# Kernel tuning notes

Hardware: AMD Instinct MI355X
Metric: run time of the kernel (lower is better)

The kernel has to match this reference:

```python
import jax, jax.numpy as jnp
import numpy as np

D_MODEL, D_K, D_V = 1024, 128, 128
B, S = 4, 4096

def setup_inputs() -> dict:
    key = jax.random.key(0)
    ks = jax.random.split(key, 9)
    sq = 1.0 / np.sqrt(D_MODEL)
    return {
        "q": jax.random.normal(ks[0], (B, S, D_MODEL), jnp.float32),
        "k": jax.random.normal(ks[1], (B, S, D_MODEL), jnp.float32),
        "v": jax.random.normal(ks[2], (B, S, D_MODEL), jnp.float32),
        "wq": jax.random.uniform(ks[3], (D_MODEL, D_K), jnp.float32, -sq, sq),
        "bq": jax.random.uniform(ks[4], (D_K,), jnp.float32, -sq, sq),
        "wk": jax.random.uniform(ks[5], (D_MODEL, D_K), jnp.float32, -sq, sq),
        "bk": jax.random.uniform(ks[6], (D_K,), jnp.float32, -sq, sq),
        "wv": jax.random.uniform(ks[7], (D_MODEL, D_V), jnp.float32, -sq, sq),
        "bv": jax.random.uniform(ks[8], (D_V,), jnp.float32, -sq, sq),
    }

def reference(q, k, v, wq, bq, wk, bk, wv, bv):
    scale = 1.0 / jnp.sqrt(jnp.asarray(D_K, q.dtype))
    qp = q @ wq + bq            # [B,S,Dk]
    kp = k @ wk + bk            # [B,S,Dk]
    vp = v @ wv + bv            # [B,S,Dv]
    scores = jnp.einsum('bqd,bkd->bqk', qp, kp) * scale  # [B,S,S]
    attn = jax.nn.softmax(scores, axis=-1)
    return jnp.einsum('bqk,bkd->bqd', attn, vp)          # [B,S,Dv]
```

## Files before the change

kernel.cpp:

```cpp
#include <hip/hip_runtime.h>
#include <stdint.h>

#define DM 1024
#define DK 128
#define SEQ 4096
#define NB 4
#define NSPLIT 4
#define KSPAN (SEQ / NSPLIT)
#define NQT (SEQ / 128)

typedef float f32x4 __attribute__((ext_vector_type(4)));
typedef float f32x16 __attribute__((ext_vector_type(16)));
typedef __bf16 bf16x8 __attribute__((ext_vector_type(8)));
typedef unsigned short u16x8 __attribute__((ext_vector_type(8)));
typedef unsigned short u16x4 __attribute__((ext_vector_type(4)));

__device__ __forceinline__ unsigned short f2bf(float f) {
    unsigned int u = __builtin_bit_cast(unsigned int, f);
    u += 0x7fffu + ((u >> 16) & 1u);
    return (unsigned short)(u >> 16);
}
__device__ __forceinline__ float bf2f(unsigned short h) {
    unsigned int u = ((unsigned int)h) << 16;
    return __builtin_bit_cast(float, u);
}
__device__ __forceinline__ f32x4 mfma16(u16x8 a, u16x8 b, f32x4 c) {
    return __builtin_amdgcn_mfma_f32_16x16x32_bf16(
        __builtin_bit_cast(bf16x8, a), __builtin_bit_cast(bf16x8, b), c, 0, 0, 0);
}
__device__ __forceinline__ f32x16 mfma32(u16x8 a, u16x8 b, f32x16 c) {
    return __builtin_amdgcn_mfma_f32_32x32x16_bf16(
        __builtin_bit_cast(bf16x8, a), __builtin_bit_cast(bf16x8, b), c, 0, 0, 0);
}

__device__ __forceinline__ bf16x8 cvt84(f32x4 lo, f32x4 hi) {
    bf16x8 r;
    r[0] = (__bf16)lo[0]; r[1] = (__bf16)lo[1]; r[2] = (__bf16)lo[2]; r[3] = (__bf16)lo[3];
    r[4] = (__bf16)hi[0]; r[5] = (__bf16)hi[1]; r[6] = (__bf16)hi[2]; r[7] = (__bf16)hi[3];
    return r;
}

__device__ __forceinline__ void gll16(const void* g, void* l) {
    __builtin_amdgcn_global_load_lds(
        (const __attribute__((address_space(1))) unsigned int*)(uintptr_t)g,
        (__attribute__((address_space(3))) unsigned int*)(uintptr_t)l,
        16, 0, 0);
}

__global__ __launch_bounds__(256) void wt_kernel(
        const float* __restrict__ wq, const float* __restrict__ wk,
        const float* __restrict__ wv, unsigned short* __restrict__ wT) {
    __shared__ unsigned short T[64 * 72];
    const int kt = blockIdx.x, dt = blockIdx.y, mat = blockIdx.z;
    const float* src = (mat == 0) ? wq : (mat == 1 ? wk : wv);
    const int tid = threadIdx.x;
    const int rb = tid >> 4, c4 = (tid & 15) * 4;
    float4 x[4];
#pragma unroll
    for (int i = 0; i < 4; i++)
        x[i] = *(const float4*)&src[(size_t)(kt * 64 + i * 16 + rb) * DK + dt * 64 + c4];
#pragma unroll
    for (int i = 0; i < 4; i++) {
        const int row = i * 16 + rb;
        T[(c4 + 0) * 72 + row] = f2bf(x[i].x);
        T[(c4 + 1) * 72 + row] = f2bf(x[i].y);
        T[(c4 + 2) * 72 + row] = f2bf(x[i].z);
        T[(c4 + 3) * 72 + row] = f2bf(x[i].w);
    }
    __syncthreads();
    const int dl = tid >> 2, ks0 = (tid & 3) * 16;
    unsigned short* dst = wT + (size_t)mat * DM * DK + (size_t)(dt * 64 + dl) * DM + kt * 64 + ks0;
#pragma unroll
    for (int j = 0; j < 2; j++)
        *(u16x8*)&dst[8 * j] = *(const u16x8*)&T[dl * 72 + ks0 + 8 * j];
}

__global__ __launch_bounds__(256)
void proj_kernel(
        const float* __restrict__ qin, const float* __restrict__ kin,
        const float* __restrict__ vin, const unsigned short* __restrict__ wT,
        const float* __restrict__ bq, const float* __restrict__ bk,
        const float* __restrict__ bv,
        unsigned short* __restrict__ qp, unsigned short* __restrict__ kp,
        unsigned short* __restrict__ vpT) {
    __shared__ __align__(16) char smem[64 * 64 * 4 + 128 * 64 * 2];
    float* Xs = (float*)smem;
    unsigned short* Ws = (unsigned short*)(smem + 64 * 64 * 4);

    const int y = blockIdx.y;
    const float* X = (y == 0) ? qin : (y == 1 ? kin : vin);
    const unsigned short* WTm = wT + (size_t)y * (DM * DK);
    const float* bias = (y == 0) ? bq : (y == 1 ? bk : bv);

    const int tid = threadIdx.x;
    const int w = tid >> 6, lane = tid & 63, l16 = lane & 15, quad = lane >> 4;
    const int t0 = blockIdx.x * 64;

    const int lr4 = lane >> 4, h16 = lane & 15;
    const int lr8 = lane >> 3, h8 = lane & 7;
    const float* xsrc[4];
    const unsigned short* wsrc[4];
    float* xdst[4];
    unsigned short* wdst[4];
#pragma unroll
    for (int i = 0; i < 4; i++) {
        const int xrow = w * 16 + i * 4 + lr4;
        const int xcol = (((h16 >> 1) ^ (xrow & 7)) << 3) |
                         (((h16 & 1) ^ ((xrow >> 3) & 1)) << 2);
        xsrc[i] = X + (size_t)(t0 + xrow) * DM + xcol;
        xdst[i] = Xs + (w * 16 + i * 4) * 64;
        const int wrow = w * 32 + i * 8 + lr8;
        const int wcol = (h8 ^ lr8) << 3;
        wsrc[i] = WTm + (size_t)wrow * DM + wcol;
        wdst[i] = Ws + (w * 32 + i * 8) * 64;
    }

    f32x4 zero = {0.f, 0.f, 0.f, 0.f};
    f32x4 acc[4][2];
#pragma unroll
    for (int mf = 0; mf < 4; mf++)
#pragma unroll
        for (int nf = 0; nf < 2; nf++) acc[mf][nf] = zero;

#pragma unroll
    for (int i = 0; i < 4; i++) { gll16(xsrc[i], xdst[i]); gll16(wsrc[i], wdst[i]); }

    const int swz = l16 & 7, h3 = (l16 >> 3) & 1;
    for (int t = 0; t < 16; ++t) {
        __syncthreads();
#pragma unroll
        for (int ks = 0; ks < 2; ks++) {
            const int ca = ((ks << 2) | quad) ^ swz;
            bf16x8 av[4];
            u16x8 bvf[2];
#pragma unroll
            for (int mf = 0; mf < 4; mf++) {
                const float* ap = &Xs[(l16 + 16 * mf) * 64 + ca * 8];
                f32x4 lo = *(const f32x4*)(ap + 4 * h3);
                f32x4 hi = *(const f32x4*)(ap + 4 * (h3 ^ 1));
                av[mf] = cvt84(lo, hi);
            }
#pragma unroll
            for (int nf = 0; nf < 2; nf++)
                bvf[nf] = *(const u16x8*)&Ws[(32 * w + 16 * nf + l16) * 64 + ca * 8];
#pragma unroll
            for (int mf = 0; mf < 4; mf++)
#pragma unroll
                for (int nf = 0; nf < 2; nf++)
                    acc[mf][nf] = __builtin_amdgcn_mfma_f32_16x16x32_bf16(
                        av[mf], __builtin_bit_cast(bf16x8, bvf[nf]), acc[mf][nf], 0, 0, 0);
        }
        __syncthreads();
        if (t < 15) {
#pragma unroll
            for (int i = 0; i < 4; i++) {
                xsrc[i] += 64;
                wsrc[i] += 64;
                gll16(xsrc[i], xdst[i]);
                gll16(wsrc[i], wdst[i]);
            }
        }
    }

    if (y < 2) {
        unsigned short* outp = y ? kp : qp;
#pragma unroll
        for (int nf = 0; nf < 2; nf++) {
            const int n = l16 + 32 * w + 16 * nf;
            const float bb = bias[n];
#pragma unroll
            for (int mf = 0; mf < 4; mf++)
#pragma unroll
                for (int r = 0; r < 4; r++)
                    outp[(size_t)(t0 + 16 * mf + quad * 4 + r) * DK + n] = f2bf(acc[mf][nf][r] + bb);
        }
    } else {
        __syncthreads();
        unsigned short* Tb = (unsigned short*)smem;
#pragma unroll
        for (int nf = 0; nf < 2; nf++) {
            const int d = l16 + 32 * w + 16 * nf;
            const float bb = bias[d];
#pragma unroll
            for (int mf = 0; mf < 4; mf++)
#pragma unroll
                for (int r = 0; r < 4; r++)
                    Tb[d * 72 + 16 * mf + quad * 4 + r] = f2bf(acc[mf][nf][r] + bb);
        }
        __syncthreads();
        const int d2 = tid >> 1, ts = (tid & 1) * 32;
        const int b2 = t0 >> 12, tl0 = t0 & (SEQ - 1);
#pragma unroll
        for (int j = 0; j < 4; j++)
            *(u16x8*)&vpT[((size_t)(b2 * DK + d2)) * SEQ + tl0 + ts + 8 * j] =
                *(const u16x8*)&Tb[d2 * 72 + ts + 8 * j];
    }
}

__global__ __launch_bounds__(256)
__attribute__((amdgpu_waves_per_eu(2, 2)))
void attn_part_kernel(
        const unsigned short* __restrict__ qp, const unsigned short* __restrict__ kp,
        const unsigned short* __restrict__ vpT,
        unsigned short* __restrict__ Opart, float* __restrict__ Lw) {
    __shared__ unsigned short Ks[64 * 136];
    __shared__ unsigned short Vs[128 * 72];

    const int tid = threadIdx.x;
    const int w = tid >> 6, lane = tid & 63, l32 = lane & 31, h = lane >> 5;
    const int qt = blockIdx.x, pi = blockIdx.y, b = blockIdx.z;
    const int q0 = qt * 128;
    const int kbase = pi * KSPAN;
    const float csc = 0.08838834764831845f * 1.4426950408889634f;

    u16x8 qf[8];
    {
        const unsigned short* qrow = qp + (size_t)(b * SEQ + q0 + 32 * w + l32) * DK + 8 * h;
#pragma unroll
        for (int c = 0; c < 8; c++) qf[c] = *(const u16x8*)&qrow[16 * c];
    }

    f32x16 oacc[4];
#pragma unroll
    for (int i = 0; i < 4; i++)
#pragma unroll
        for (int j = 0; j < 16; j++) oacc[i][j] = 0.f;
    float l_acc = 0.f;

    const int krow = tid >> 2, kch = (tid & 3) * 8;
    const int vrow = tid >> 1, voff = (tid & 1) * 8;
    uint4 kbuf[4], vbuf[4];
    {
        const unsigned short* kg = kp + (size_t)(b * SEQ + kbase + krow) * DK + kch;
        const unsigned short* vg = vpT + (size_t)(b * DK + vrow) * SEQ + kbase + voff;
#pragma unroll
        for (int i = 0; i < 4; i++) {
            kbuf[i] = *(const uint4*)&kg[32 * i];
            vbuf[i] = *(const uint4*)&vg[16 * i];
        }
    }

    for (int it = 0; it < KSPAN / 64; it++) {
        __syncthreads();
#pragma unroll
        for (int i = 0; i < 4; i++) {
            *(u16x8*)&Ks[krow * 136 + kch + 32 * i] = __builtin_bit_cast(u16x8, kbuf[i]);
            *(u16x8*)&Vs[vrow * 72 + voff + 16 * i] = __builtin_bit_cast(u16x8, vbuf[i]);
        }
        __syncthreads();
        if (it + 1 < KSPAN / 64) {
            const int kn = kbase + (it + 1) * 64;
            const unsigned short* kg = kp + (size_t)(b * SEQ + kn + krow) * DK + kch;
            const unsigned short* vg = vpT + (size_t)(b * DK + vrow) * SEQ + kn + voff;
#pragma unroll
            for (int i = 0; i < 4; i++) {
                kbuf[i] = *(const uint4*)&kg[32 * i];
                vbuf[i] = *(const uint4*)&vg[16 * i];
            }
        }
        f32x16 sacc[2];
#pragma unroll
        for (int kb = 0; kb < 2; kb++)
#pragma unroll
            for (int j = 0; j < 16; j++) sacc[kb][j] = 0.f;
#pragma unroll
        for (int c = 0; c < 8; c++)
#pragma unroll
            for (int kb = 0; kb < 2; kb++) {
                u16x8 kf = *(const u16x8*)&Ks[(l32 + 32 * kb) * 136 + 16 * c + 8 * h];
                sacc[kb] = mfma32(kf, qf[c], sacc[kb]);
            }
        unsigned int pp[16];
#pragma unroll
        for (int kb = 0; kb < 2; kb++)
#pragma unroll
            for (int r2 = 0; r2 < 8; r2++) {
                float p0 = exp2f(sacc[kb][2 * r2] * csc);
                float p1 = exp2f(sacc[kb][2 * r2 + 1] * csc);
                l_acc += p0 + p1;
                pp[kb * 8 + r2] = (unsigned int)f2bf(p0) | ((unsigned int)f2bf(p1) << 16);
            }
#pragma unroll
        for (int c = 0; c < 4; c++) {
            const int bs = (c >> 1) * 8 + (c & 1) * 4;
            unsigned int o0 = pp[bs], o1 = pp[bs + 1], o2 = pp[bs + 2], o3 = pp[bs + 3];
            unsigned int x0 = __shfl_xor(o0, 32), x1 = __shfl_xor(o1, 32);
            unsigned int x2 = __shfl_xor(o2, 32), x3 = __shfl_xor(o3, 32);
            uint4 af;
            af.x = h ? x2 : o0;
            af.y = h ? x3 : o1;
            af.z = h ? o2 : x0;
            af.w = h ? o3 : x1;
            u16x8 afr = __builtin_bit_cast(u16x8, af);
#pragma unroll
            for (int db = 0; db < 4; db++) {
                u16x8 vf = *(const u16x8*)&Vs[(32 * db + l32) * 72 + 16 * c + 8 * h];
                oacc[db] = mfma32(afr, vf, oacc[db]);
            }
        }
    }
    float l_tot = l_acc + __shfl_xor(l_acc, 32);
    if (lane < 32)
        Lw[(size_t)(b * NSPLIT + pi) * SEQ + q0 + 32 * w + l32] = l_tot;
    float rl[16];
#pragma unroll
    for (int r = 0; r < 16; r++) {
        int qr = (r & 3) + 8 * (r >> 2) + 4 * h;
        rl[r] = 1.f / __shfl(l_tot, qr);
    }
    unsigned short* ob = Opart + ((size_t)((b * NSPLIT + pi) * NQT + qt)) * 16384 + (size_t)tid * 64;
#pragma unroll
    for (int db = 0; db < 4; db++) {
        u16x8 s0, s1;
#pragma unroll
        for (int j = 0; j < 8; j++) {
            s0[j] = f2bf(oacc[db][j] * rl[j]);
            s1[j] = f2bf(oacc[db][8 + j] * rl[8 + j]);
        }
        *(u16x8*)&ob[db * 16] = s0;
        *(u16x8*)&ob[db * 16 + 8] = s1;
    }
}

__global__ __launch_bounds__(256) void attn_combine_kernel(
        const unsigned short* __restrict__ Opart, const float* __restrict__ Lw,
        float* __restrict__ out) {
    __shared__ float Ls[NSPLIT * 128];
    const int tid = threadIdx.x;
    const int w = tid >> 6, lane = tid & 63, l32 = lane & 31, h = lane >> 5;
    const int qt = blockIdx.x, b = blockIdx.y, z = blockIdx.z;
    const int q0 = qt * 128;
    for (int i = tid; i < NSPLIT * 128; i += 256) {
        int pi = i >> 7, ql = i & 127;
        Ls[i] = Lw[(size_t)(b * NSPLIT + pi) * SEQ + q0 + ql];
    }
    __syncthreads();
    int qlr[16];
    float inv[16];
#pragma unroll
    for (int r = 0; r < 16; r++) {
        qlr[r] = 32 * w + (r & 3) + 8 * (r >> 2) + 4 * h;
        float s = 0.f;
#pragma unroll
        for (int pi = 0; pi < NSPLIT; pi++) s += Ls[pi * 128 + qlr[r]];
        inv[r] = 1.f / s;
    }
    float acc[32];
#pragma unroll
    for (int i = 0; i < 32; i++) acc[i] = 0.f;
#pragma unroll
    for (int pi = 0; pi < NSPLIT; pi++) {
        float wr[16];
#pragma unroll
        for (int r = 0; r < 16; r++) wr[r] = Ls[pi * 128 + qlr[r]] * inv[r];
        const unsigned short* ob =
            Opart + ((size_t)((b * NSPLIT + pi) * NQT + qt)) * 16384 + (size_t)tid * 64;
#pragma unroll
        for (int j = 0; j < 2; j++) {
            const int db = 2 * z + j;
#pragma unroll
            for (int hf = 0; hf < 2; hf++) {
                u16x8 v8 = *(const u16x8*)&ob[db * 16 + 8 * hf];
#pragma unroll
                for (int jj = 0; jj < 8; jj++)
                    acc[j * 16 + 8 * hf + jj] += wr[8 * hf + jj] * bf2f(v8[jj]);
            }
        }
    }
#pragma unroll
    for (int j = 0; j < 2; j++) {
        const int db = 2 * z + j;
#pragma unroll
        for (int r = 0; r < 16; r++)
            out[(size_t)(b * SEQ + q0 + qlr[r]) * DK + 32 * db + l32] = acc[j * 16 + r];
    }
}

extern "C" void kernel_launch(void* const* d_in, const int* in_sizes, int n_in,
                              void* d_out, int out_size, void* d_ws, size_t ws_size,
                              hipStream_t stream) {
    const float* q  = (const float*)d_in[0];
    const float* k  = (const float*)d_in[1];
    const float* v  = (const float*)d_in[2];
    const float* wq = (const float*)d_in[3];
    const float* bq = (const float*)d_in[4];
    const float* wk = (const float*)d_in[5];
    const float* bk = (const float*)d_in[6];
    const float* wv = (const float*)d_in[7];
    const float* bv = (const float*)d_in[8];
    float* out = (float*)d_out;

    char* ws = (char*)d_ws;
    unsigned short* wT    = (unsigned short*)(ws);
    unsigned short* qp    = (unsigned short*)(ws + (1u << 20));
    unsigned short* kpb   = (unsigned short*)(ws + (5u << 20));
    unsigned short* vpT   = (unsigned short*)(ws + (9u << 20));
    unsigned short* Opart = (unsigned short*)(ws + (13u << 20));
    float* Lw             = (float*)(ws + (29u << 20));

    hipLaunchKernelGGL(wt_kernel, dim3(16, 2, 3), dim3(256), 0, stream, wq, wk, wv, wT);
    hipLaunchKernelGGL(proj_kernel, dim3(256, 3), dim3(256), 0, stream,
                       q, k, v, wT, bq, bk, bv, qp, kpb, vpT);
    hipLaunchKernelGGL(attn_part_kernel, dim3(NQT, NSPLIT, NB), dim3(256), 0, stream,
                       qp, kpb, vpT, Opart, Lw);
    hipLaunchKernelGGL(attn_combine_kernel, dim3(NQT, NB, 2), dim3(256), 0, stream,
                       Opart, Lw, out);
}
```

Baseline: 286.9 us.

## Double-buffer LDS tiles in projection GEMM to overlap loads with MFMA

```diff
diff --git a/kernel.cpp b/kernel.cpp
--- a/kernel.cpp
+++ b/kernel.cpp
@@ -83,9 +83,7 @@
         const float* __restrict__ bv,
         unsigned short* __restrict__ qp, unsigned short* __restrict__ kp,
         unsigned short* __restrict__ vpT) {
-    __shared__ __align__(16) char smem[64 * 64 * 4 + 128 * 64 * 2];
-    float* Xs = (float*)smem;
-    unsigned short* Ws = (unsigned short*)(smem + 64 * 64 * 4);
+    __shared__ __align__(16) char smem[2 * 32768];
 
     const int y = blockIdx.y;
     const float* X = (y == 0) ? qin : (y == 1 ? kin : vin);
@@ -100,20 +98,30 @@
     const int lr8 = lane >> 3, h8 = lane & 7;
     const float* xsrc[4];
     const unsigned short* wsrc[4];
-    float* xdst[4];
-    unsigned short* wdst[4];
+    int xdo[4], wdo[4];
 #pragma unroll
     for (int i = 0; i < 4; i++) {
         const int xrow = w * 16 + i * 4 + lr4;
         const int xcol = (((h16 >> 1) ^ (xrow & 7)) << 3) |
                          (((h16 & 1) ^ ((xrow >> 3) & 1)) << 2);
         xsrc[i] = X + (size_t)(t0 + xrow) * DM + xcol;
-        xdst[i] = Xs + (w * 16 + i * 4) * 64;
+        xdo[i] = (w * 16 + i * 4) * 64 * 4;
         const int wrow = w * 32 + i * 8 + lr8;
         const int wcol = (h8 ^ lr8) << 3;
         wsrc[i] = WTm + (size_t)wrow * DM + wcol;
-        wdst[i] = Ws + (w * 32 + i * 8) * 64;
-    }
+        wdo[i] = 16384 + (w * 32 + i * 8) * 64 * 2;
+    }
+
+#define PROJ_STAGE(B)                                          \
+    do {                                                       \
+        char* _base = smem + (B) * 32768;                      \
+        _Pragma("unroll") for (int _i = 0; _i < 4; _i++) {     \
+            gll16(xsrc[_i], _base + xdo[_i]);                  \
+            gll16(wsrc[_i], _base + wdo[_i]);                  \
+            xsrc[_i] += 64;                                    \
+            wsrc[_i] += 64;                                    \
+        }                                                      \
+    } while (0)
 
     f32x4 zero = {0.f, 0.f, 0.f, 0.f};
     f32x4 acc[4][2];
@@ -122,44 +130,47 @@
 #pragma unroll
         for (int nf = 0; nf < 2; nf++) acc[mf][nf] = zero;
 
-#pragma unroll
-    for (int i = 0; i < 4; i++) { gll16(xsrc[i], xdst[i]); gll16(wsrc[i], wdst[i]); }
-
     const int swz = l16 & 7, h3 = (l16 >> 3) & 1;
-    for (int t = 0; t < 16; ++t) {
-        __syncthreads();
-#pragma unroll
-        for (int ks = 0; ks < 2; ks++) {
-            const int ca = ((ks << 2) | quad) ^ swz;
-            bf16x8 av[4];
-            u16x8 bvf[2];
-#pragma unroll
-            for (int mf = 0; mf < 4; mf++) {
-                const float* ap = &Xs[(l16 + 16 * mf) * 64 + ca * 8];
-                f32x4 lo = *(const f32x4*)(ap + 4 * h3);
-                f32x4 hi = *(const f32x4*)(ap + 4 * (h3 ^ 1));
-                av[mf] = cvt84(lo, hi);
-            }
-#pragma unroll
-            for (int nf = 0; nf < 2; nf++)
-                bvf[nf] = *(const u16x8*)&Ws[(32 * w + 16 * nf + l16) * 64 + ca * 8];
-#pragma unroll
-            for (int mf = 0; mf < 4; mf++)
-#pragma unroll
-                for (int nf = 0; nf < 2; nf++)
-                    acc[mf][nf] = __builtin_amdgcn_mfma_f32_16x16x32_bf16(
-                        av[mf], __builtin_bit_cast(bf16x8, bvf[nf]), acc[mf][nf], 0, 0, 0);
-        }
-        __syncthreads();
-        if (t < 15) {
-#pragma unroll
-            for (int i = 0; i < 4; i++) {
-                xsrc[i] += 64;
-                wsrc[i] += 64;
-                gll16(xsrc[i], xdst[i]);
-                gll16(wsrc[i], wdst[i]);
-            }
-        }
+
+#define PROJ_COMPUTE(B)                                                          \
+    do {                                                                         \
+        const float* _Xb = (const float*)(smem + (B) * 32768);                   \
+        const unsigned short* _Wb = (const unsigned short*)(smem + (B) * 32768 + 16384); \
+        _Pragma("unroll") for (int ks = 0; ks < 2; ks++) {                       \
+            const int ca = ((ks << 2) | quad) ^ swz;                             \
+            bf16x8 av[4];                                                        \
+            u16x8 bvf[2];                                                        \
+            _Pragma("unroll") for (int mf = 0; mf < 4; mf++) {                   \
+                const float* ap = &_Xb[(l16 + 16 * mf) * 64 + ca * 8];           \
+                f32x4 lo = *(const f32x4*)(ap + 4 * h3);                         \
+                f32x4 hi = *(const f32x4*)(ap + 4 * (h3 ^ 1));                   \
+                av[mf] = cvt84(lo, hi);                                          \
+            }                                                                    \
+            _Pragma("unroll") for (int nf = 0; nf < 2; nf++)                     \
+                bvf[nf] = *(const u16x8*)&_Wb[(32 * w + 16 * nf + l16) * 64 + ca * 8]; \
+            _Pragma("unroll") for (int mf = 0; mf < 4; mf++)                     \
+                _Pragma("unroll") for (int nf = 0; nf < 2; nf++)                 \
+                    acc[mf][nf] = __builtin_amdgcn_mfma_f32_16x16x32_bf16(       \
+                        av[mf], __builtin_bit_cast(bf16x8, bvf[nf]),             \
+                        acc[mf][nf], 0, 0, 0);                                   \
+        }                                                                        \
+    } while (0)
+
+#define PROJ_WAITBAR()                                     \
+    do {                                                   \
+        asm volatile("s_waitcnt vmcnt(0)" ::: "memory");   \
+        __builtin_amdgcn_s_barrier();                      \
+    } while (0)
+
+    PROJ_STAGE(0);
+    PROJ_WAITBAR();
+    for (int s = 0; s < 16; s += 2) {
+        PROJ_STAGE(1);
+        PROJ_COMPUTE(0);
+        PROJ_WAITBAR();
+        if (s + 2 < 16) PROJ_STAGE(0);
+        PROJ_COMPUTE(1);
+        PROJ_WAITBAR();
     }
 
     if (y < 2) {
@@ -195,6 +206,9 @@
             *(u16x8*)&vpT[((size_t)(b2 * DK + d2)) * SEQ + tl0 + ts + 8 * j] =
                 *(const u16x8*)&Tb[d2 * 72 + ts + 8 * j];
     }
+#undef PROJ_STAGE
+#undef PROJ_COMPUTE
+#undef PROJ_WAITBAR
 }
 
 __global__ __launch_bounds__(256)
```

After: 289.3 us. Within noise of the previous version (+0.8%).
